# Optimization experiments

Hardware: AMD Instinct MI355X
Metric: run time of the kernel (lower is better)

The kernel has to match this reference:

```python
import jax, jax.numpy as jnp
import numpy as np

N, K, M = 1024, 256, 1024
INIT_SCALE = 0.1


def setup_inputs() -> dict:
    key = jax.random.key(0)
    kx, kw = jax.random.split(key)
    x = jax.random.normal(kx, (N, K), dtype=jnp.float32)
    weight = jax.random.normal(kw, (M, K), dtype=jnp.float32) * INIT_SCALE
    return {"x": x, "weight": weight}


def reference(x, weight):
    # Tropical (max-plus) matmul: out[n, m] = max_k(|x[n, k]| + |w[m, k]|)
    ax = jnp.abs(x)        # [N, K]
    aw = jnp.abs(weight)   # [M, K]
    # broadcast to [N, M, K] then reduce over K (mirrors the original expand+add+max)
    return jnp.max(ax[:, None, :] + aw[None, :, :], axis=2)  # [N, M]
```

## Files before the change

kernel.cpp:

```cpp
#include <hip/hip_runtime.h>


typedef float v2f __attribute__((ext_vector_type(2)));
typedef float v4f __attribute__((ext_vector_type(4)));

constexpr int K   = 256;
constexpr int M   = 1024;
constexpr int KC  = 64;
constexpr int NCH = K / KC;
constexpr int WP  = 68;

__global__ void __launch_bounds__(256, 4)
tropical_kernel(const float* __restrict__ xg, const float* __restrict__ wg,
                float* __restrict__ outg)
{
    __shared__ __align__(16) float wlds[64 * WP];

    const int tid  = threadIdx.x;
    const int lane = tid & 63;
    const int wv   = __builtin_amdgcn_readfirstlane(tid >> 6);

    const int bn = (int)(blockIdx.x >> 4) * 16;
    const int bm = (int)(blockIdx.x & 15) * 64;

    const int wrow = tid >> 2;
    const int wcol = (tid & 3) * 16;
    const float* wbase = wg + (bm + wrow) * K + wcol;

    v4f pref[4];
#pragma unroll
    for (int i = 0; i < 4; ++i) pref[i] = *(const v4f*)(wbase + 4 * i);

    float acc[4] = {0.f, 0.f, 0.f, 0.f};

    const float* xrow0 = xg + (bn + 4 * wv) * K;

    for (int c = 0; c < NCH; ++c) {
        __syncthreads();
#pragma unroll
        for (int i = 0; i < 4; ++i) {
            v4f t = pref[i];
            *(v4f*)&wlds[wrow * WP + wcol + 4 * i] =
                (v4f){fabsf(t.x), fabsf(t.y), fabsf(t.z), fabsf(t.w)};
        }
        if (c + 1 < NCH) {
#pragma unroll
            for (int i = 0; i < 4; ++i)
                pref[i] = *(const v4f*)(wbase + (c + 1) * KC + 4 * i);
        }
        __syncthreads();

        v2f wreg[KC / 2];
#pragma unroll
        for (int q = 0; q < KC / 4; ++q) {
            v4f t = *(const v4f*)&wlds[lane * WP + 4 * q];
            wreg[2 * q]     = (v2f){t.x, t.y};
            wreg[2 * q + 1] = (v2f){t.z, t.w};
        }

#pragma unroll
        for (int jn = 0; jn < 4; ++jn) {
            const float* xr = xrow0 + jn * K + c * KC;
#pragma unroll
            for (int kp = 0; kp < KC / 2; ++kp) {
                v2f xu = (v2f){fabsf(xr[2 * kp]), fabsf(xr[2 * kp + 1])};
                v2f s  = wreg[kp] + xu;
                acc[jn] = fmaxf(acc[jn], fmaxf(s.x, s.y));
            }
        }
    }

#pragma unroll
    for (int jn = 0; jn < 4; ++jn)
        outg[(bn + 4 * wv + jn) * M + bm + lane] = acc[jn];
}

extern "C" void kernel_launch(void* const* d_in, const int* in_sizes, int n_in,
                              void* d_out, int out_size, void* d_ws, size_t ws_size,
                              hipStream_t stream)
{
    const float* x = (const float*)d_in[0];
    const float* w = (const float*)d_in[1];
    float* out = (float*)d_out;

    dim3 grid(1024);
    dim3 block(256);
    tropical_kernel<<<grid, block, 0, stream>>>(x, w, out);
}
```

Measured before the change: 78.11 us.

## Drop LDS staging, load weights per lane, widen block tile to 64 rows

Removes the shared-memory staging of the weight tile and its two barriers per chunk. Each lane now reads its own weight row straight from global memory into registers, with a register prefetch of the next 32-wide chunk. Blocks grow to 512 threads covering 64 x-rows, each wave handling 8 rows, and the grid shrinks to 256 blocks. x values are loaded as 64-bit pairs with a bitmask absolute value. The risks are uncoalesced strided weight loads (each lane reads a different row), higher register pressure from 8 accumulators, and fewer blocks to fill the GPU.

```diff
diff --git a/kernel.cpp b/kernel.cpp
--- a/kernel.cpp
+++ b/kernel.cpp
@@ -1,78 +1,75 @@
 #include <hip/hip_runtime.h>
+#include <stdint.h>
 
 
 typedef float v2f __attribute__((ext_vector_type(2)));
 typedef float v4f __attribute__((ext_vector_type(4)));
 
-constexpr int K   = 256;
-constexpr int M   = 1024;
-constexpr int KC  = 64;
+constexpr int K  = 256;
+constexpr int M  = 1024;
+constexpr int KC = 32;
 constexpr int NCH = K / KC;
-constexpr int WP  = 68;
 
-__global__ void __launch_bounds__(256, 4)
+static __device__ inline v2f abs2(double d) {
+    uint64_t b = __builtin_bit_cast(uint64_t, d) & 0x7FFFFFFF7FFFFFFFULL;
+    return __builtin_bit_cast(v2f, b);
+}
+
+__global__ void __launch_bounds__(512)
 tropical_kernel(const float* __restrict__ xg, const float* __restrict__ wg,
                 float* __restrict__ outg)
 {
-    __shared__ __align__(16) float wlds[64 * WP];
-
     const int tid  = threadIdx.x;
     const int lane = tid & 63;
     const int wv   = __builtin_amdgcn_readfirstlane(tid >> 6);
 
-    const int bn = (int)(blockIdx.x >> 4) * 16;
+    const int bn = (int)(blockIdx.x >> 4) * 64;
     const int bm = (int)(blockIdx.x & 15) * 64;
 
-    const int wrow = tid >> 2;
-    const int wcol = (tid & 3) * 16;
-    const float* wbase = wg + (bm + wrow) * K + wcol;
+    const float* wrow = wg + (bm + lane) * K;
+    const int n0 = bn + 8 * wv;
+    const float* xrow = xg + n0 * K;
 
-    v4f pref[4];
+    float acc[8];
 #pragma unroll
-    for (int i = 0; i < 4; ++i) pref[i] = *(const v4f*)(wbase + 4 * i);
+    for (int j = 0; j < 8; ++j) acc[j] = 0.0f;
 
-    float acc[4] = {0.f, 0.f, 0.f, 0.f};
-
-    const float* xrow0 = xg + (bn + 4 * wv) * K;
+    v4f wf[KC / 4];
+#pragma unroll
+    for (int q = 0; q < KC / 4; ++q) wf[q] = *(const v4f*)(wrow + 4 * q);
 
     for (int c = 0; c < NCH; ++c) {
-        __syncthreads();
+        v2f wa[KC / 2];
 #pragma unroll
-        for (int i = 0; i < 4; ++i) {
-            v4f t = pref[i];
-            *(v4f*)&wlds[wrow * WP + wcol + 4 * i] =
-                (v4f){fabsf(t.x), fabsf(t.y), fabsf(t.z), fabsf(t.w)};
+        for (int q = 0; q < KC / 4; ++q) {
+            v4f t = wf[q];
+            wa[2 * q]     = (v2f){fabsf(t.x), fabsf(t.y)};
+            wa[2 * q + 1] = (v2f){fabsf(t.z), fabsf(t.w)};
         }
         if (c + 1 < NCH) {
 #pragma unroll
-            for (int i = 0; i < 4; ++i)
-                pref[i] = *(const v4f*)(wbase + (c + 1) * KC + 4 * i);
-        }
-        __syncthreads();
-
-        v2f wreg[KC / 2];
-#pragma unroll
-        for (int q = 0; q < KC / 4; ++q) {
-            v4f t = *(const v4f*)&wlds[lane * WP + 4 * q];
-            wreg[2 * q]     = (v2f){t.x, t.y};
-            wreg[2 * q + 1] = (v2f){t.z, t.w};
+            for (int q = 0; q < KC / 4; ++q)
+                wf[q] = *(const v4f*)(wrow + (c + 1) * KC + 4 * q);
         }
 
 #pragma unroll
-        for (int jn = 0; jn < 4; ++jn) {
-            const float* xr = xrow0 + jn * K + c * KC;
+        for (int j = 0; j < 8; ++j) {
+            const double* xr = (const double*)(xrow + j * K + c * KC);
+            double xb[KC / 2];
+#pragma unroll
+            for (int kp = 0; kp < KC / 2; ++kp) xb[kp] = xr[kp];
 #pragma unroll
             for (int kp = 0; kp < KC / 2; ++kp) {
-                v2f xu = (v2f){fabsf(xr[2 * kp]), fabsf(xr[2 * kp + 1])};
-                v2f s  = wreg[kp] + xu;
-                acc[jn] = fmaxf(acc[jn], fmaxf(s.x, s.y));
+                v2f xu = abs2(xb[kp]);
+                v2f s  = wa[kp] + xu;
+                acc[j] = fmaxf(acc[j], fmaxf(s.x, s.y));
             }
         }
     }
 
 #pragma unroll
-    for (int jn = 0; jn < 4; ++jn)
-        outg[(bn + 4 * wv + jn) * M + bm + lane] = acc[jn];
+    for (int j = 0; j < 8; ++j)
+        outg[(n0 + j) * M + bm + lane] = acc[j];
 }
 
 extern "C" void kernel_launch(void* const* d_in, const int* in_sizes, int n_in,
@@ -83,7 +80,7 @@
     const float* w = (const float*)d_in[1];
     float* out = (float*)d_out;
 
-    dim3 grid(1024);
-    dim3 block(256);
+    dim3 grid(256);
+    dim3 block(512);
     tropical_kernel<<<grid, block, 0, stream>>>(x, w, out);
 }
```

After: 97.33 us. 24.6% more time.
